# Performance work log

Measured on AMD Instinct MI355X. Metric: run time of the kernel, lower is better.

Reference implementation:

```python
import jax, jax.numpy as jnp
import numpy as np

STRIDE, PADDING, EPS = 2, 1, 1e-5


def setup_inputs() -> dict:
    key = jax.random.key(0)
    k1, k2, k3 = jax.random.split(key, 3)
    C_in, C_out, K = 64, 64, 4
    x = jax.random.normal(k1, (32, C_in, 64, 64), dtype=jnp.float32)
    weight = jax.random.normal(k2, (C_in, C_out, K, K), dtype=jnp.float32) * 0.05  # torch layout (in,out,kh,kw)
    conv_bias = jax.random.normal(k3, (C_out,), dtype=jnp.float32) * 0.02
    gamma = jnp.ones((C_out,), dtype=jnp.float32)
    beta = jnp.zeros((C_out,), dtype=jnp.float32)
    running_mean = jnp.zeros((C_out,), dtype=jnp.float32)
    running_var = jnp.ones((C_out,), dtype=jnp.float32)
    return {"x": x, "weight": weight, "conv_bias": conv_bias, "gamma": gamma,
            "beta": beta, "running_mean": running_mean, "running_var": running_var}


def _conv_transpose2d(x, weight, bias, stride, padding):
    # torch.nn.functional.conv_transpose2d equivalent:
    # conv with lhs_dilation=stride, spatially-flipped kernel, in/out axes swapped,
    # and padding k-1-p on each side.
    k = weight.shape[2]
    w_t = jnp.transpose(jnp.flip(weight, (2, 3)), (1, 0, 2, 3))  # (Cout, Cin, k, k)
    pad = k - 1 - padding
    y = jax.lax.conv_general_dilated(
        x, w_t,
        window_strides=(1, 1),
        padding=[(pad, pad), (pad, pad)],
        lhs_dilation=(stride, stride),
        dimension_numbers=("NCHW", "OIHW", "NCHW"),
    )
    return y + bias[None, :, None, None]


def reference(x, weight, conv_bias, gamma, beta, running_mean, running_var):
    # ConvTranspose2d
    y = _conv_transpose2d(x, weight, conv_bias, STRIDE, PADDING)  # [N,C,128,128]
    # BatchNorm2d (inference, running stats)
    scale = gamma * jax.lax.rsqrt(running_var + EPS)
    y = (y - running_mean[None, :, None, None]) * scale[None, :, None, None] + beta[None, :, None, None]
    # Softmax over channel dim
    y = jax.nn.softmax(y, axis=1)
    # MaxPool2d(k=2, s=2): H,W are even, so reshape-max is exact
    N, C, H, W = y.shape
    y = y.reshape(N, C, H // 2, 2, W // 2, 2).max(axis=(3, 5))  # [N,C,64,64]
    return y
```

## Files before the change

### kernel.cpp

```cpp
#include <hip/hip_runtime.h>
#include <math.h>


typedef __attribute__((ext_vector_type(8))) short short8;
typedef __attribute__((ext_vector_type(4))) float floatx4;

#define PITCH 72
#define COLS 66

__device__ ushort g_wfrag[4 * 8 * 4 * 64 * 8];
__device__ float g_aff[128];

__device__ __forceinline__ ushort f2bf(float f) {
  union { float f; unsigned u; } v; v.f = f;
  unsigned r = v.u + 0x7FFF + ((v.u >> 16) & 1);
  return (ushort)(r >> 16);
}

__global__ __launch_bounds__(256) void prep_kernel(
    const float* __restrict__ w, const float* __restrict__ bias,
    const float* __restrict__ gamma, const float* __restrict__ beta,
    const float* __restrict__ mean, const float* __restrict__ var) {
  int tid = blockIdx.x * 256 + threadIdx.x;
  for (int e = tid; e < 4 * 8 * 4 * 64 * 8; e += 64 * 256) {
    int j    = e & 7;
    int lane = (e >> 3) & 63;
    int nt   = (e >> 9) & 3;
    int ks   = (e >> 11) & 7;
    int c    = (e >> 14) & 3;
    int k    = ks * 32 + (lane >> 4) * 8 + j;
    int tap  = k >> 6, cin = k & 63;
    int cout = nt * 16 + (lane & 15);
    int r = c >> 1, p = c & 1;
    int a = tap >> 1, b = tap & 1;
    int kh = r ? (a ? 2 : 0) : (a ? 3 : 1);
    int kw = p ? (b ? 2 : 0) : (b ? 3 : 1);
    g_wfrag[e] = f2bf(w[(cin * 64 + cout) * 16 + kh * 4 + kw]);
  }
  if (blockIdx.x == 0 && threadIdx.x < 64) {
    int c = threadIdx.x;
    float A = gamma[c] * rsqrtf(var[c] + 1e-5f);
    g_aff[c] = A;
    g_aff[64 + c] = (bias[c] - mean[c]) * A + beta[c];
  }
}

__global__ __launch_bounds__(256) void fused_kernel(const float* __restrict__ x,
                                                    float* __restrict__ out) {
  __shared__ ushort xs[3 * COLS * PITCH];

  const int tid  = threadIdx.x;
  const int ph   = blockIdx.x;
  const int n    = blockIdx.y;
  const int wave = tid >> 6;
  const int lane = tid & 63;
  const int b15  = lane & 15;
  const int q    = lane >> 4;

  for (int e = tid; e < 3 * 16 * 64; e += 256) {
    int iw  = e & 63;
    int c4  = (e >> 6) & 15;
    int row = e >> 10;
    int ih  = ph - 1 + row;
    int cin = c4 * 4;
    float v0 = 0.f, v1 = 0.f, v2 = 0.f, v3 = 0.f;
    if (ih >= 0 && ih < 64) {
      const float* xp = x + ((n * 64 + cin) * 64 + ih) * 64 + iw;
      v0 = xp[0]; v1 = xp[4096]; v2 = xp[8192]; v3 = xp[12288];
    }
    ushort4 pk;
    pk.x = f2bf(v0); pk.y = f2bf(v1); pk.z = f2bf(v2); pk.w = f2bf(v3);
    *(ushort4*)&xs[(row * COLS + iw + 1) * PITCH + cin] = pk;
  }
  for (int e = tid; e < 3 * 2 * 16; e += 256) {
    int c4  = e & 15;
    int side = (e >> 4) & 1;
    int row = e >> 5;
    ushort4 z; z.x = z.y = z.z = z.w = 0;
    *(ushort4*)&xs[(row * COLS + (side ? 65 : 0)) * PITCH + c4 * 4] = z;
  }
  __syncthreads();

  float Ac[4], Dc[4];
#pragma unroll
  for (int nt = 0; nt < 4; ++nt) {
    Ac[nt] = g_aff[nt * 16 + b15];
    Dc[nt] = g_aff[64 + nt * 16 + b15];
  }

  float pooled[16];
#pragma unroll
  for (int i = 0; i < 16; ++i) pooled[i] = 0.f;

#pragma unroll
  for (int c = 0; c < 4; ++c) {
    const int r = c >> 1, p = c & 1;
    floatx4 acc[4];
#pragma unroll
    for (int nt = 0; nt < 4; ++nt) acc[nt] = (floatx4){0.f, 0.f, 0.f, 0.f};

#pragma unroll
    for (int ks = 0; ks < 8; ++ks) {
      const int tap = ks >> 1, a = tap >> 1, b = tap & 1;
      const int row = r ? (a ? 1 : 2) : (a ? 0 : 1);
      const int dx  = p ? (b ? 0 : 1) : (b ? -1 : 0);
      const int col = wave * 16 + b15 + dx + 1;
      const int cin0 = (ks & 1) * 32 + q * 8;
      short8 afrag = *(const short8*)&xs[(row * COLS + col) * PITCH + cin0];
      const short8* wf = (const short8*)&g_wfrag[((c * 8 + ks) * 4 * 64 + lane) * 8];
#pragma unroll
      for (int nt = 0; nt < 4; ++nt) {
        short8 bfrag = wf[nt * 64];
        acc[nt] = __builtin_amdgcn_mfma_f32_16x16x32_bf16(afrag, bfrag, acc[nt], 0, 0, 0);
      }
    }

    float v[16], mx[4], sm[4];
#pragma unroll
    for (int reg = 0; reg < 4; ++reg) mx[reg] = -1e30f;
#pragma unroll
    for (int nt = 0; nt < 4; ++nt)
#pragma unroll
      for (int reg = 0; reg < 4; ++reg) {
        float y = fmaf(acc[nt][reg], Ac[nt], Dc[nt]);
        v[nt * 4 + reg] = y;
        mx[reg] = fmaxf(mx[reg], y);
      }
#pragma unroll
    for (int reg = 0; reg < 4; ++reg) {
      mx[reg] = fmaxf(mx[reg], __shfl_xor(mx[reg], 1, 64));
      mx[reg] = fmaxf(mx[reg], __shfl_xor(mx[reg], 2, 64));
      mx[reg] = fmaxf(mx[reg], __shfl_xor(mx[reg], 4, 64));
      mx[reg] = fmaxf(mx[reg], __shfl_xor(mx[reg], 8, 64));
      sm[reg] = 0.f;
    }
#pragma unroll
    for (int nt = 0; nt < 4; ++nt)
#pragma unroll
      for (int reg = 0; reg < 4; ++reg) {
        float e = __expf(v[nt * 4 + reg] - mx[reg]);
        v[nt * 4 + reg] = e;
        sm[reg] += e;
      }
#pragma unroll
    for (int reg = 0; reg < 4; ++reg) {
      sm[reg] += __shfl_xor(sm[reg], 1, 64);
      sm[reg] += __shfl_xor(sm[reg], 2, 64);
      sm[reg] += __shfl_xor(sm[reg], 4, 64);
      sm[reg] += __shfl_xor(sm[reg], 8, 64);
      sm[reg] = 1.0f / sm[reg];
    }
#pragma unroll
    for (int nt = 0; nt < 4; ++nt)
#pragma unroll
      for (int reg = 0; reg < 4; ++reg)
        pooled[nt * 4 + reg] =
            fmaxf(pooled[nt * 4 + reg], v[nt * 4 + reg] * sm[reg]);
  }

  __syncthreads();
  float* red = (float*)xs;
#pragma unroll
  for (int nt = 0; nt < 4; ++nt)
#pragma unroll
    for (int reg = 0; reg < 4; ++reg) {
      int cout = nt * 16 + b15;
      int pw   = wave * 16 + q * 4 + reg;
      red[cout * 66 + pw] = pooled[nt * 4 + reg];
    }
  __syncthreads();
  for (int e = tid; e < 2048; e += 256) {
    int pwh  = e & 31;
    int cout = e >> 5;
    float2 val = *(float2*)&red[cout * 66 + pwh * 2];
    *(float2*)&out[((n * 64 + cout) * 64 + ph) * 64 + pwh * 2] = val;
  }
}

extern "C" void kernel_launch(void* const* d_in, const int* in_sizes, int n_in,
                              void* d_out, int out_size, void* d_ws, size_t ws_size,
                              hipStream_t stream) {
  const float* x     = (const float*)d_in[0];
  const float* w     = (const float*)d_in[1];
  const float* bias  = (const float*)d_in[2];
  const float* gamma = (const float*)d_in[3];
  const float* beta  = (const float*)d_in[4];
  const float* mean  = (const float*)d_in[5];
  const float* var   = (const float*)d_in[6];
  float* out = (float*)d_out;

  prep_kernel<<<64, 256, 0, stream>>>(w, bias, gamma, beta, mean, var);
  dim3 grid(64, 32);
  fused_kernel<<<grid, 256, 0, stream>>>(x, out);
}
```

Before: 139.3 us.

## Process four output rows per block with register-tiled MFMA and vectorized loads

Each block now handles four pooled rows instead of one. Each wave owns one row and loops over four 16-column M tiles, so every weight fragment loaded from global memory is reused across four MFMAs and the input halo rows are shared across rows. The max-subtraction pass in the softmax is dropped, which relies on the logits being small enough not to overflow exp. Input staging switches to float2 loads, the prep kernel writes packed 16-byte fragments, and the grid shrinks to 512 blocks with more registers per thread, so occupancy and wave parallelism drop.

```diff
diff --git a/kernel.cpp b/kernel.cpp
--- a/kernel.cpp
+++ b/kernel.cpp
@@ -21,61 +21,66 @@
     const float* __restrict__ w, const float* __restrict__ bias,
     const float* __restrict__ gamma, const float* __restrict__ beta,
     const float* __restrict__ mean, const float* __restrict__ var) {
-  int tid = blockIdx.x * 256 + threadIdx.x;
-  for (int e = tid; e < 4 * 8 * 4 * 64 * 8; e += 64 * 256) {
-    int j    = e & 7;
-    int lane = (e >> 3) & 63;
-    int nt   = (e >> 9) & 3;
-    int ks   = (e >> 11) & 7;
-    int c    = (e >> 14) & 3;
-    int k    = ks * 32 + (lane >> 4) * 8 + j;
-    int tap  = k >> 6, cin = k & 63;
-    int cout = nt * 16 + (lane & 15);
-    int r = c >> 1, p = c & 1;
+  int idx = blockIdx.x * 256 + threadIdx.x;
+  int lane = idx & 63;
+  int nt   = (idx >> 6) & 3;
+  int ks   = (idx >> 8) & 7;
+  int c    = (idx >> 11) & 3;
+  int r = c >> 1, p = c & 1;
+  int cout = nt * 16 + (lane & 15);
+  ushort u[8];
+#pragma unroll
+  for (int j = 0; j < 8; ++j) {
+    int k   = ks * 32 + (lane >> 4) * 8 + j;
+    int tap = k >> 6, cin = k & 63;
     int a = tap >> 1, b = tap & 1;
     int kh = r ? (a ? 2 : 0) : (a ? 3 : 1);
     int kw = p ? (b ? 2 : 0) : (b ? 3 : 1);
-    g_wfrag[e] = f2bf(w[(cin * 64 + cout) * 16 + kh * 4 + kw]);
-  }
+    u[j] = f2bf(w[(cin * 64 + cout) * 16 + kh * 4 + kw]);
+  }
+  int4 pk;
+  pk.x = u[0] | (u[1] << 16); pk.y = u[2] | (u[3] << 16);
+  pk.z = u[4] | (u[5] << 16); pk.w = u[6] | (u[7] << 16);
+  *(int4*)&g_wfrag[idx * 8] = pk;
   if (blockIdx.x == 0 && threadIdx.x < 64) {
-    int c = threadIdx.x;
-    float A = gamma[c] * rsqrtf(var[c] + 1e-5f);
-    g_aff[c] = A;
-    g_aff[64 + c] = (bias[c] - mean[c]) * A + beta[c];
-  }
-}
-
-__global__ __launch_bounds__(256) void fused_kernel(const float* __restrict__ x,
-                                                    float* __restrict__ out) {
-  __shared__ ushort xs[3 * COLS * PITCH];
+    int ch = threadIdx.x;
+    float A = gamma[ch] * rsqrtf(var[ch] + 1e-5f);
+    g_aff[ch] = A;
+    g_aff[64 + ch] = (bias[ch] - mean[ch]) * A + beta[ch];
+  }
+}
+
+__global__ __launch_bounds__(256, 2) void fused_kernel(const float* __restrict__ x,
+                                                       float* __restrict__ out) {
+  __shared__ ushort xs[6 * COLS * PITCH];
 
   const int tid  = threadIdx.x;
-  const int ph   = blockIdx.x;
+  const int ph0  = blockIdx.x * 4;
   const int n    = blockIdx.y;
   const int wave = tid >> 6;
   const int lane = tid & 63;
   const int b15  = lane & 15;
   const int q    = lane >> 4;
 
-  for (int e = tid; e < 3 * 16 * 64; e += 256) {
-    int iw  = e & 63;
-    int c4  = (e >> 6) & 15;
-    int row = e >> 10;
-    int ih  = ph - 1 + row;
-    int cin = c4 * 4;
-    float v0 = 0.f, v1 = 0.f, v2 = 0.f, v3 = 0.f;
+  for (int e = tid; e < 6 * 16 * 32; e += 256) {
+    int iw2 = e & 31;
+    int c4  = (e >> 5) & 15;
+    int row = e >> 9;
+    int ih  = ph0 - 1 + row;
+    float2 v0 = {0.f, 0.f}, v1 = v0, v2 = v0, v3 = v0;
     if (ih >= 0 && ih < 64) {
-      const float* xp = x + ((n * 64 + cin) * 64 + ih) * 64 + iw;
-      v0 = xp[0]; v1 = xp[4096]; v2 = xp[8192]; v3 = xp[12288];
-    }
-    ushort4 pk;
-    pk.x = f2bf(v0); pk.y = f2bf(v1); pk.z = f2bf(v2); pk.w = f2bf(v3);
-    *(ushort4*)&xs[(row * COLS + iw + 1) * PITCH + cin] = pk;
-  }
-  for (int e = tid; e < 3 * 2 * 16; e += 256) {
-    int c4  = e & 15;
-    int side = (e >> 4) & 1;
-    int row = e >> 5;
+      const float* xp = x + ((n * 64 + c4 * 4) * 64 + ih) * 64 + iw2 * 2;
+      v0 = *(const float2*)xp;         v1 = *(const float2*)(xp + 4096);
+      v2 = *(const float2*)(xp + 8192); v3 = *(const float2*)(xp + 12288);
+    }
+    ushort4 pa, pb;
+    pa.x = f2bf(v0.x); pa.y = f2bf(v1.x); pa.z = f2bf(v2.x); pa.w = f2bf(v3.x);
+    pb.x = f2bf(v0.y); pb.y = f2bf(v1.y); pb.z = f2bf(v2.y); pb.w = f2bf(v3.y);
+    *(ushort4*)&xs[(row * COLS + iw2 * 2 + 1) * PITCH + c4 * 4] = pa;
+    *(ushort4*)&xs[(row * COLS + iw2 * 2 + 2) * PITCH + c4 * 4] = pb;
+  }
+  for (int e = tid; e < 6 * 2 * 16; e += 256) {
+    int c4 = e & 15, side = (e >> 4) & 1, row = e >> 5;
     ushort4 z; z.x = z.y = z.z = z.w = 0;
     *(ushort4*)&xs[(row * COLS + (side ? 65 : 0)) * PITCH + c4 * 4] = z;
   }
@@ -88,92 +93,92 @@
     Dc[nt] = g_aff[64 + nt * 16 + b15];
   }
 
-  float pooled[16];
-#pragma unroll
-  for (int i = 0; i < 16; ++i) pooled[i] = 0.f;
+  floatx4 pooled[16];
+#pragma unroll
+  for (int i = 0; i < 16; ++i) pooled[i] = (floatx4){0.f, 0.f, 0.f, 0.f};
 
 #pragma unroll
   for (int c = 0; c < 4; ++c) {
     const int r = c >> 1, p = c & 1;
-    floatx4 acc[4];
-#pragma unroll
-    for (int nt = 0; nt < 4; ++nt) acc[nt] = (floatx4){0.f, 0.f, 0.f, 0.f};
+    floatx4 acc[16];
+#pragma unroll
+    for (int i = 0; i < 16; ++i) acc[i] = (floatx4){0.f, 0.f, 0.f, 0.f};
 
 #pragma unroll
     for (int ks = 0; ks < 8; ++ks) {
       const int tap = ks >> 1, a = tap >> 1, b = tap & 1;
-      const int row = r ? (a ? 1 : 2) : (a ? 0 : 1);
-      const int dx  = p ? (b ? 0 : 1) : (b ? -1 : 0);
-      const int col = wave * 16 + b15 + dx + 1;
+      const int hrow = wave + (r ? (a ? 1 : 2) : (a ? 0 : 1));
+      const int dx   = p ? (b ? 0 : 1) : (b ? -1 : 0);
       const int cin0 = (ks & 1) * 32 + q * 8;
-      short8 afrag = *(const short8*)&xs[(row * COLS + col) * PITCH + cin0];
+      const ushort* xrow = &xs[(hrow * COLS + 1 + dx + b15) * PITCH + cin0];
+      short8 af[4];
+#pragma unroll
+      for (int mt = 0; mt < 4; ++mt)
+        af[mt] = *(const short8*)&xrow[mt * 16 * PITCH];
       const short8* wf = (const short8*)&g_wfrag[((c * 8 + ks) * 4 * 64 + lane) * 8];
 #pragma unroll
       for (int nt = 0; nt < 4; ++nt) {
-        short8 bfrag = wf[nt * 64];
-        acc[nt] = __builtin_amdgcn_mfma_f32_16x16x32_bf16(afrag, bfrag, acc[nt], 0, 0, 0);
+        short8 bf = wf[nt * 64];
+#pragma unroll
+        for (int mt = 0; mt < 4; ++mt)
+          acc[mt * 4 + nt] =
+              __builtin_amdgcn_mfma_f32_16x16x32_bf16(af[mt], bf, acc[mt * 4 + nt], 0, 0, 0);
       }
     }
 
-    float v[16], mx[4], sm[4];
-#pragma unroll
-    for (int reg = 0; reg < 4; ++reg) mx[reg] = -1e30f;
-#pragma unroll
-    for (int nt = 0; nt < 4; ++nt)
+#pragma unroll
+    for (int mt = 0; mt < 4; ++mt) {
+      float v[16];
+      float sm[4] = {0.f, 0.f, 0.f, 0.f};
+#pragma unroll
+      for (int nt = 0; nt < 4; ++nt)
+#pragma unroll
+        for (int reg = 0; reg < 4; ++reg) {
+          float e = __expf(fmaf(acc[mt * 4 + nt][reg], Ac[nt], Dc[nt]));
+          v[nt * 4 + reg] = e;
+          sm[reg] += e;
+        }
 #pragma unroll
       for (int reg = 0; reg < 4; ++reg) {
-        float y = fmaf(acc[nt][reg], Ac[nt], Dc[nt]);
-        v[nt * 4 + reg] = y;
-        mx[reg] = fmaxf(mx[reg], y);
+        sm[reg] += __shfl_xor(sm[reg], 1, 64);
+        sm[reg] += __shfl_xor(sm[reg], 2, 64);
+        sm[reg] += __shfl_xor(sm[reg], 4, 64);
+        sm[reg] += __shfl_xor(sm[reg], 8, 64);
+        sm[reg] = 1.0f / sm[reg];
       }
 #pragma unroll
-    for (int reg = 0; reg < 4; ++reg) {
-      mx[reg] = fmaxf(mx[reg], __shfl_xor(mx[reg], 1, 64));
-      mx[reg] = fmaxf(mx[reg], __shfl_xor(mx[reg], 2, 64));
-      mx[reg] = fmaxf(mx[reg], __shfl_xor(mx[reg], 4, 64));
-      mx[reg] = fmaxf(mx[reg], __shfl_xor(mx[reg], 8, 64));
-      sm[reg] = 0.f;
-    }
-#pragma unroll
-    for (int nt = 0; nt < 4; ++nt)
-#pragma unroll
-      for (int reg = 0; reg < 4; ++reg) {
-        float e = __expf(v[nt * 4 + reg] - mx[reg]);
-        v[nt * 4 + reg] = e;
-        sm[reg] += e;
-      }
-#pragma unroll
-    for (int reg = 0; reg < 4; ++reg) {
-      sm[reg] += __shfl_xor(sm[reg], 1, 64);
-      sm[reg] += __shfl_xor(sm[reg], 2, 64);
-      sm[reg] += __shfl_xor(sm[reg], 4, 64);
-      sm[reg] += __shfl_xor(sm[reg], 8, 64);
-      sm[reg] = 1.0f / sm[reg];
-    }
-#pragma unroll
-    for (int nt = 0; nt < 4; ++nt)
-#pragma unroll
-      for (int reg = 0; reg < 4; ++reg)
-        pooled[nt * 4 + reg] =
-            fmaxf(pooled[nt * 4 + reg], v[nt * 4 + reg] * sm[reg]);
+      for (int nt = 0; nt < 4; ++nt)
+#pragma unroll
+        for (int reg = 0; reg < 4; ++reg)
+          pooled[mt * 4 + nt][reg] =
+              fmaxf(pooled[mt * 4 + nt][reg], v[nt * 4 + reg] * sm[reg]);
+    }
   }
 
   __syncthreads();
   float* red = (float*)xs;
 #pragma unroll
-  for (int nt = 0; nt < 4; ++nt)
-#pragma unroll
-    for (int reg = 0; reg < 4; ++reg) {
-      int cout = nt * 16 + b15;
-      int pw   = wave * 16 + q * 4 + reg;
-      red[cout * 66 + pw] = pooled[nt * 4 + reg];
-    }
-  __syncthreads();
-  for (int e = tid; e < 2048; e += 256) {
-    int pwh  = e & 31;
-    int cout = e >> 5;
-    float2 val = *(float2*)&red[cout * 66 + pwh * 2];
-    *(float2*)&out[((n * 64 + cout) * 64 + ph) * 64 + pwh * 2] = val;
+  for (int pp = 0; pp < 2; ++pp) {
+    if ((wave >> 1) == pp) {
+      int rl = wave & 1;
+#pragma unroll
+      for (int nt = 0; nt < 4; ++nt)
+#pragma unroll
+        for (int mt = 0; mt < 4; ++mt)
+#pragma unroll
+          for (int reg = 0; reg < 4; ++reg)
+            red[(rl * 64 + nt * 16 + b15) * 66 + mt * 16 + q * 4 + reg] =
+                pooled[mt * 4 + nt][reg];
+    }
+    __syncthreads();
+    for (int e = tid; e < 4096; e += 256) {
+      int pw2  = e & 31;
+      int cout = (e >> 5) & 63;
+      int rl   = e >> 11;
+      float2 val = *(float2*)&red[(rl * 64 + cout) * 66 + pw2 * 2];
+      *(float2*)&out[((n * 64 + cout) * 64 + (ph0 + pp * 2 + rl)) * 64 + pw2 * 2] = val;
+    }
+    __syncthreads();
   }
 }
 
@@ -189,7 +194,7 @@
   const float* var   = (const float*)d_in[6];
   float* out = (float*)d_out;
 
-  prep_kernel<<<64, 256, 0, stream>>>(w, bias, gamma, beta, mean, var);
-  dim3 grid(64, 32);
+  prep_kernel<<<32, 256, 0, stream>>>(w, bias, gamma, beta, mean, var);
+  dim3 grid(16, 32);
   fused_kernel<<<grid, 256, 0, stream>>>(x, out);
 }
```

Result: slower. 166.5 us (+19.6%).
